# Performance work log

Measured on AMD Instinct MI355X. Metric: run time of the kernel, lower is better.

Reference implementation:

```python
import jax, jax.numpy as jnp
import numpy as np

EPS = 1e-6
NEG = -10000.0

def compute_alibi_slopes(n_head):
    # standard ALiBi slopes for power-of-two head counts: 2^{-8(i+1)/n}
    start = 2.0 ** (-8.0 / n_head)
    return jnp.asarray([start ** (i + 1) for i in range(n_head)], dtype=jnp.float32)

def setup_inputs() -> dict:
    key = jax.random.key(0)
    k1, k2, k3 = jax.random.split(key, 3)
    B, T, C, H = 2, 2048, 1024, 16
    x = jax.random.normal(k1, (B, T, C), dtype=jnp.float32)
    # torch nn.Linear weights are [out_features, in_features]
    w_qkv = jax.random.normal(k2, (3 * C, C), dtype=jnp.float32) * (C ** -0.5)
    w_out = jax.random.normal(k3, (C, C), dtype=jnp.float32) * (C ** -0.5)
    alibi_slopes = compute_alibi_slopes(H)
    return {"x": x, "w_qkv": w_qkv, "w_out": w_out, "alibi_slopes": alibi_slopes}

def rational_softmax(scores, eps=EPS):
    # algebraic sigmoid 0.5*(1 + x/sqrt(1+x^2)) normalized along last axis
    num = 0.5 * (1.0 + scores * jax.lax.rsqrt(1.0 + scores * scores))
    return num / (jnp.sum(num, axis=-1, keepdims=True) + eps)

def reference(x, w_qkv, w_out, alibi_slopes):
    B, T, C = x.shape
    H = alibi_slopes.shape[0]
    D = C // H
    scale = 1.0 / jnp.sqrt(jnp.float32(D))
    qkv = (x @ w_qkv.T).reshape(B, T, 3, H, D)
    qkv = jnp.transpose(qkv, (2, 0, 3, 1, 4))  # [3,B,H,T,D]
    q, k, v = qkv[0], qkv[1], qkv[2]
    scores = jnp.einsum("bhtd,bhsd->bhts", q, k) * scale  # [B,H,T,T]
    pos = jnp.arange(T)
    rel = pos[:, None] - pos[None, :]  # [T,T]
    alibi = -jnp.abs(rel).astype(jnp.float32) * alibi_slopes[None, :, None, None]
    scores = scores + alibi
    causal = rel < 0  # strictly upper triangle (j > i)
    scores = jnp.where(causal[None, None], NEG, scores)
    probs = rational_softmax(scores, EPS)
    out = jnp.einsum("bhts,bhsd->bhtd", probs, v)  # [B,H,T,D]
    out = jnp.transpose(out, (0, 2, 1, 3)).reshape(B, T, C)
    return out @ w_out.T
```

## Files before the change

kernel.cpp:

```cpp
#include <hip/hip_runtime.h>
#include <stdint.h>

typedef __attribute__((ext_vector_type(8))) short bf16x8;
typedef __attribute__((ext_vector_type(4))) float f32x4;
typedef __attribute__((ext_vector_type(16))) float f32x16;

#define MFMA_16x16x32(a, b, c) __builtin_amdgcn_mfma_f32_16x16x32_bf16((a), (b), (c), 0, 0, 0)
#define MFMA_32x32x16(a, b, c) __builtin_amdgcn_mfma_f32_32x32x16_bf16((a), (b), (c), 0, 0, 0)

__device__ __forceinline__ short f2bf(float f) {
  union { float f; uint32_t u; } x;
  x.f = f;
  uint32_t r = x.u + 0x7fffu + ((x.u >> 16) & 1u);
  return (short)(r >> 16);
}

__device__ __forceinline__ uint32_t cvt_pk_bf16(float lo, float hi) {
  uint32_t r;
  asm("v_cvt_pk_bf16_f32 %0, %1, %2" : "=v"(r) : "v"(lo), "v"(hi));
  return r;
}

__device__ __forceinline__ void gload_lds16(const short* g, short* l) {
  __builtin_amdgcn_global_load_lds(
      (const __attribute__((address_space(1))) void*)g,
      (__attribute__((address_space(3))) void*)l, 16, 0, 0);
}

__global__ __launch_bounds__(256) void cast_all(const float* __restrict__ x,
                                                const float* __restrict__ wq,
                                                const float* __restrict__ wo,
                                                short* __restrict__ xb,
                                                short* __restrict__ wqb,
                                                short* __restrict__ wob) {
  int i = blockIdx.x * 256 + threadIdx.x;
  const float* s;
  short* d;
  int off;
  float sc = 1.0f;
  if (i < 524288) { s = x; d = xb; off = i; }
  else if (i < 917504) {
    s = wq; d = wqb; off = i - 524288;
    if (off < 131072) sc = 0.125f;
  }
  else { s = wo; d = wob; off = i - 917504; }
  const float4* sp = (const float4*)s;
  float4 v0 = sp[(size_t)off * 2 + 0];
  float4 v1 = sp[(size_t)off * 2 + 1];
  bf16x8 o;
  o[0] = f2bf(v0.x * sc); o[1] = f2bf(v0.y * sc); o[2] = f2bf(v0.z * sc); o[3] = f2bf(v0.w * sc);
  o[4] = f2bf(v1.x * sc); o[5] = f2bf(v1.y * sc); o[6] = f2bf(v1.z * sc); o[7] = f2bf(v1.w * sc);
  *(bf16x8*)(d + (size_t)off * 8) = o;
}

template <int OUT_BF16>
__global__ __launch_bounds__(512, 2) void gemm256(const short* __restrict__ A,
                                                  const short* __restrict__ B,
                                                  void* __restrict__ Cp,
                                                  int M, int N, int K, int ntN) {
  __shared__ short Al[2][2][128 * 64];
  __shared__ short Bl[2][2][128 * 64];

  const int tid = threadIdx.x;
  const int wv = tid >> 6, lane = tid & 63;
  const int wr = wv >> 2, wc = wv & 3;
  const int lrow = lane & 15, kgrp = lane >> 4;
  const int l3 = lrow & 7;
  const int ck0 = ((kgrp ^ l3)) * 8;
  const int ck1 = ((kgrp ^ l3) ^ 4) * 8;

  const int nwg = gridDim.x;
  const int orig = blockIdx.x;
  const int wg = (orig & 7) * (nwg >> 3) + (orig >> 3);
  const int by = wg / ntN, bx = wg % ntN;
  const int row0 = by * 256, col0 = bx * 256;

  const int r_ = tid >> 3;
  const int cs_ = ((tid & 7) ^ (r_ & 7)) * 8;

  const int NT = K >> 6;
  const int NI = NT >> 1;
  const int NTm1 = NT - 1;

  auto stgA = [&](int slot, int h, int j, int kt) {
    gload_lds16(A + (size_t)(row0 + h * 128 + j * 64 + r_) * K + kt * 64 + cs_,
                &Al[slot][h][j * 4096 + wv * 512]);
  };
  auto stgB = [&](int slot, int h, int j, int kt) {
    gload_lds16(B + (size_t)(col0 + h * 128 + j * 64 + r_) * K + kt * 64 + cs_,
                &Bl[slot][h][j * 4096 + wv * 512]);
  };

  f32x4 acc[8][4] = {};

  const int boff = ((wc & 1) * 64 + lrow) * 64;
  const int bh = wc >> 1;

  stgB(0, 0, 0, 0); stgB(0, 0, 1, 0); stgB(0, 1, 0, 0); stgB(0, 1, 1, 0);
  stgA(0, 0, 0, 0); stgA(0, 0, 1, 0); stgA(0, 1, 0, 0); stgA(0, 1, 1, 0);
  stgB(1, 0, 0, 1); stgB(1, 0, 1, 1); stgB(1, 1, 0, 1); stgB(1, 1, 1, 1);
  asm volatile("s_waitcnt vmcnt(4)" ::: "memory");
  __builtin_amdgcn_s_barrier();

  for (int i = 0; i < NI; ++i) {
    const int ktB1 = (2 * i + 1);
    const int ktP2 = (2 * i + 2 > NTm1) ? NTm1 : 2 * i + 2;
    const int ktP3 = (2 * i + 3 > NTm1) ? NTm1 : 2 * i + 3;
#pragma unroll
    for (int s = 0; s < 2; ++s) {
      bf16x8 bfr[4][2];
#pragma unroll
      for (int q = 0; q < 4; ++q) {
        if (q == 0) {
#pragma unroll
          for (int n = 0; n < 4; ++n) {
            bfr[n][0] = *(const bf16x8*)(&Bl[s][bh][boff + n * 1024 + ck0]);
            bfr[n][1] = *(const bf16x8*)(&Bl[s][bh][boff + n * 1024 + ck1]);
          }
        }
        bf16x8 afr[2][2];
#pragma unroll
        for (int mm = 0; mm < 2; ++mm) {
          const int m = q * 2 + mm;
          afr[mm][0] = *(const bf16x8*)(&Al[s][wr][lrow * 64 + m * 1024 + ck0]);
          afr[mm][1] = *(const bf16x8*)(&Al[s][wr][lrow * 64 + m * 1024 + ck1]);
        }
        if (s == 0) {
          if (q == 0) { stgA(1, 0, 0, ktB1); stgA(1, 0, 1, ktB1); stgA(1, 1, 0, ktB1); stgA(1, 1, 1, ktB1); }
          else if (q == 1) { stgB(0, 0, 0, ktP2); stgB(0, 0, 1, ktP2); }
          else if (q == 2) { stgB(0, 1, 0, ktP2); stgB(0, 1, 1, ktP2); }
        } else {
          if (q == 0) { stgA(0, 0, 0, ktP2); stgA(0, 0, 1, ktP2); stgA(0, 1, 0, ktP2); stgA(0, 1, 1, ktP2); }
          else if (q == 1) { stgB(1, 0, 0, ktP3); stgB(1, 0, 1, ktP3); }
          else if (q == 2) { stgB(1, 1, 0, ktP3); stgB(1, 1, 1, ktP3); }
        }
        __builtin_amdgcn_sched_barrier(0);
        __builtin_amdgcn_s_barrier();
        asm volatile("s_waitcnt lgkmcnt(0)" ::: "memory");
        __builtin_amdgcn_sched_barrier(0);
        __builtin_amdgcn_s_setprio(1);
#pragma unroll
        for (int mm = 0; mm < 2; ++mm)
#pragma unroll
          for (int n = 0; n < 4; ++n)
#pragma unroll
            for (int kk = 0; kk < 2; ++kk)
              acc[q * 2 + mm][n] = MFMA_16x16x32(afr[mm][kk], bfr[n][kk], acc[q * 2 + mm][n]);
        __builtin_amdgcn_s_setprio(0);
        __builtin_amdgcn_sched_barrier(0);
        if (q == 3) {
          asm volatile("s_waitcnt vmcnt(4)" ::: "memory");
        }
        __builtin_amdgcn_s_barrier();
      }
    }
  }

  asm volatile("s_waitcnt vmcnt(0)" ::: "memory");

#pragma unroll
  for (int m = 0; m < 8; ++m) {
    const int grow = row0 + wr * 128 + m * 16 + kgrp * 4;
#pragma unroll
    for (int n = 0; n < 4; ++n) {
      const int gcol = col0 + wc * 64 + n * 16 + lrow;
#pragma unroll
      for (int j = 0; j < 4; ++j) {
        const size_t off = (size_t)(grow + j) * N + gcol;
        if (OUT_BF16) ((short*)Cp)[off] = f2bf(acc[m][n][j]);
        else          ((float*)Cp)[off] = acc[m][n][j];
      }
    }
  }
}

template <int OUT_BF16>
__global__ __launch_bounds__(256, 4) void gemm_bt64(const short* __restrict__ A,
                                                    const short* __restrict__ B,
                                                    void* __restrict__ Cp,
                                                    int M, int N, int K) {
  __shared__ short As[64 * 64];
  __shared__ short Bs[128 * 64];
  const int tid = threadIdx.x;
  const int wave = tid >> 6, lane = tid & 63;
  const int wr = wave >> 1, wc = wave & 1;
  const int row0 = blockIdx.y * 64, col0 = blockIdx.x * 128;
  const int lrow = lane & 15;
  const int kgrp = lane >> 4;
  const int l3 = lrow & 7;

  const int r_ = tid >> 3;
  const int cs_ = ((tid & 7) ^ (r_ & 7)) * 8;

  f32x4 acc[2][4] = {};

  for (int k0 = 0; k0 < K; k0 += 64) {
#pragma unroll
    for (int it = 0; it < 2; ++it)
      gload_lds16(A + (size_t)(row0 + it * 32 + r_) * K + k0 + cs_,
                  As + (it * 256 + wave * 64) * 8);
#pragma unroll
    for (int it = 0; it < 4; ++it)
      gload_lds16(B + (size_t)(col0 + it * 32 + r_) * K + k0 + cs_,
                  Bs + (it * 256 + wave * 64) * 8);
    __syncthreads();
#pragma unroll
    for (int kk = 0; kk < 2; ++kk) {
      const int ck = ((kk * 4 + kgrp) ^ l3) * 8;
      bf16x8 a[2], b[4];
#pragma unroll
      for (int m = 0; m < 2; ++m)
        a[m] = *(const bf16x8*)(As + (wr * 32 + m * 16 + lrow) * 64 + ck);
#pragma unroll
      for (int n = 0; n < 4; ++n)
        b[n] = *(const bf16x8*)(Bs + (wc * 64 + n * 16 + lrow) * 64 + ck);
#pragma unroll
      for (int m = 0; m < 2; ++m)
#pragma unroll
        for (int n = 0; n < 4; ++n)
          acc[m][n] = MFMA_16x16x32(a[m], b[n], acc[m][n]);
    }
    __syncthreads();
  }

#pragma unroll
  for (int m = 0; m < 2; ++m) {
    int rbase = row0 + wr * 32 + m * 16 + kgrp * 4;
#pragma unroll
    for (int n = 0; n < 4; ++n) {
      int col = col0 + wc * 64 + n * 16 + lrow;
#pragma unroll
      for (int j = 0; j < 4; ++j) {
        size_t off = (size_t)(rbase + j) * N + col;
        if (OUT_BF16) ((short*)Cp)[off] = f2bf(acc[m][n][j]);
        else          ((float*)Cp)[off] = acc[m][n][j];
      }
    }
  }
}

__global__ __launch_bounds__(256) void transpose_v(const short* __restrict__ qkv,
                                                   short* __restrict__ vt) {
  const int T = 2048;
  __shared__ short sm[64][72];
  const int bh = blockIdx.y, h = bh & 15, b = bh >> 4;
  const int t0 = blockIdx.x * 64;
  const int tid = threadIdx.x;
#pragma unroll
  for (int p = 0; p < 2; ++p) {
    int idx = p * 256 + tid;
    int tl = idx >> 3, d0 = (idx & 7) * 8;
    bf16x8 v = *(const bf16x8*)(qkv + (b * T + t0 + tl) * 3072 + 2048 + h * 64 + d0);
    *(bf16x8*)(&sm[tl][d0]) = v;
  }
  __syncthreads();
#pragma unroll
  for (int p = 0; p < 2; ++p) {
    int idx = p * 256 + tid;
    int d = idx >> 3, ts0 = (idx & 7) * 8;
    bf16x8 o;
#pragma unroll
    for (int j = 0; j < 8; ++j) o[j] = sm[ts0 + j][d];
    *(bf16x8*)(vt + (bh * 64 + d) * T + t0 + ts0) = o;
  }
}

template <bool DIAG>
__device__ __forceinline__ void attn_sub(
    const short* __restrict__ Kb, const short* __restrict__ Vb,
    const bf16x8 (&qf)[4], const f32x16& crun,
    f32x16& acc0, f32x16& acc1, float (&den4)[4],
    int l31, int hi, int shalf, int mbits) {
  const int krow = l31 >> 1;
  const int kc0 = (l31 & 1) * 8 + hi;
  const int ss = shalf;
  __builtin_amdgcn_s_setprio(1);
  const bf16x8 kf0 = *(const bf16x8*)(Kb + (ss * 16 + krow) * 128 + (kc0 ^ krow) * 8);
  f32x16 s = MFMA_32x32x16(kf0, qf[0], crun);
#pragma unroll
  for (int kkd = 1; kkd < 4; ++kkd) {
    const bf16x8 kf = *(const bf16x8*)(Kb + (ss * 16 + krow) * 128 +
                                       ((kc0 + kkd * 2) ^ krow) * 8);
    s = MFMA_32x32x16(kf, qf[kkd], s);
  }
  __builtin_amdgcn_s_setprio(0);
  float nm[16];
#pragma unroll
  for (int v = 0; v < 16; ++v) {
    float x = s[v];
    if (DIAG) x = ((mbits >> v) & 1) ? -10000.0f : x;
    float t = fmaf(x, x, 1.0f);
    float num = fmaf(x * __builtin_amdgcn_rsqf(t), 0.5f, 0.5f);
    den4[v & 3] += num;
    nm[v] = num;
  }
#pragma unroll
  for (int k1 = 0; k1 < 2; ++k1) {
    union { uint32_t u[4]; bf16x8 v8; } pu;
#pragma unroll
    for (int w01 = 0; w01 < 2; ++w01) {
      uint32_t c0 = cvt_pk_bf16(nm[2 * w01 + 8 * k1], nm[2 * w01 + 8 * k1 + 1]);
      uint32_t c1 = cvt_pk_bf16(nm[2 * w01 + 8 * k1 + 4], nm[2 * w01 + 8 * k1 + 5]);
      asm volatile("v_permlane32_swap_b32 %0, %1" : "+v"(c0), "+v"(c1));
      pu.u[w01] = c0;
      pu.u[w01 + 2] = c1;
    }
    const int vsw = ((((l31 & 1) * 8) + ss * 4 + k1 * 2 + hi) ^ krow) * 8;
    const bf16x8 vf0 = *(const bf16x8*)(Vb + krow * 128 + vsw);
    const bf16x8 vf1 = *(const bf16x8*)(Vb + (16 + krow) * 128 + vsw);
    __builtin_amdgcn_s_setprio(1);
    acc0 = MFMA_32x32x16(pu.v8, vf0, acc0);
    acc1 = MFMA_32x32x16(pu.v8, vf1, acc1);
    __builtin_amdgcn_s_setprio(0);
  }
}

__global__ __launch_bounds__(256, 3) void attn_kernel(const short* __restrict__ qkv,
                                                      const short* __restrict__ vt,
                                                      const float* __restrict__ slopes,
                                                      short* __restrict__ attn_out) {
  const int T = 2048, C = 1024, C3 = 3072;
  __shared__ short Kl[3][4096];
  __shared__ short Vl[3][4096];
  __shared__ float denm[64];

  const int tid = threadIdx.x, wv = tid >> 6, lane = tid & 63;
  const int l31 = lane & 31, hi = lane >> 5;
  const int wg = blockIdx.x;
  const int bh = (wg & 7) + ((wg >> 3) & 3) * 8;
  const int qi = 31 - (wg >> 5);
  const int b = bh >> 4, h = bh & 15;
  const int qsub = wv >> 1, shalf = wv & 1;
  const float slope = slopes[h];
  const float s64 = slope * 64.0f;

  const int W = (int)(45.0f / (64.0f * slope)) + 2;
  const int kt0 = (qi - W > 0) ? (qi - W) : 0;

  int mbits = 0;
#pragma unroll
  for (int v = 0; v < 16; ++v) {
    int s32 = (v & 3) + 8 * (v >> 2) + 4 * hi;
    if (s32 > l31) mbits |= (1 << v);
  }
  int koff[2], voff[2];
#pragma unroll
  for (int p = 0; p < 2; ++p) {
    int idx = p * 256 + tid;
    int rho = idx >> 4, u = idx & 15, c = u ^ (rho & 15);
    koff[p] = (2 * rho + (c >> 3)) * C3 + (c & 7) * 8;
    voff[p] = (2 * rho + (c >> 3)) * T + (c & 7) * 8;
  }
  const short* kbase = qkv + (size_t)b * T * C3 + C + h * 64;
  const short* vbase = vt + (size_t)bh * 64 * T;

  auto STAGE = [&](int bufi, int kt) {
#pragma unroll
    for (int p = 0; p < 2; ++p)
      gload_lds16(kbase + (size_t)kt * 64 * C3 + koff[p], &Kl[bufi][(p * 256 + wv * 64) * 8]);
#pragma unroll
    for (int p = 0; p < 2; ++p)
      gload_lds16(vbase + kt * 64 + voff[p], &Vl[bufi][(p * 256 + wv * 64) * 8]);
  };

  STAGE(0, kt0);
  STAGE(1, (kt0 + 1 > qi) ? qi : kt0 + 1);

  const int qg = qi * 64 + qsub * 32 + l31;
  bf16x8 qf[4];
#pragma unroll
  for (int ks = 0; ks < 4; ++ks)
    qf[ks] = *(const bf16x8*)(qkv + (size_t)(b * T + qg) * C3 + h * 64 + ks * 16 + hi * 8);

  f32x16 crun;
#pragma unroll
  for (int v = 0; v < 16; ++v) {
    int s32 = (v & 3) + 8 * (v >> 2) + 4 * hi;
    crun[v] = slope * (float)(s32 - l31 + 32 * (shalf - qsub) + 64 * (kt0 - qi));
  }

  f32x16 acc0 = {}, acc1 = {};
  float den4[4] = {0.f, 0.f, 0.f, 0.f};

  int cA = 0, cS = 2;
  for (int kt = kt0; kt < qi; ++kt) {
    const int kt2 = (kt + 2 > qi) ? qi : kt + 2;
    STAGE(cS, kt2);
    asm volatile("s_waitcnt vmcnt(8)" ::: "memory");
    __builtin_amdgcn_s_barrier();
    attn_sub<false>(Kl[cA], Vl[cA], qf, crun, acc0, acc1, den4, l31, hi, shalf, mbits);
#pragma unroll
    for (int v = 0; v < 16; ++v) crun[v] += s64;
    __builtin_amdgcn_s_barrier();
    cA = (cA == 2) ? 0 : cA + 1;
    cS = (cS == 2) ? 0 : cS + 1;
  }
  asm volatile("s_waitcnt vmcnt(4)" ::: "memory");
  __builtin_amdgcn_s_barrier();
  if (!(qsub == 0 && shalf == 1)) {
    if (qsub == 1 && shalf == 0)
      attn_sub<false>(Kl[cA], Vl[cA], qf, crun, acc0, acc1, den4, l31, hi, shalf, mbits);
    else
      attn_sub<true>(Kl[cA], Vl[cA], qf, crun, acc0, acc1, den4, l31, hi, shalf, mbits);
  }
  __syncthreads();

  float den = (den4[0] + den4[1]) + (den4[2] + den4[3]);
  den += __shfl_xor(den, 32);

  if (shalf == 1) {
    float* mp = (float*)(qsub == 0 ? &Kl[cS][0] : &Vl[cS][0]);
#pragma unroll
    for (int i = 0; i < 16; ++i) {
      mp[i * 64 + lane] = acc0[i];
      mp[(16 + i) * 64 + lane] = acc1[i];
    }
    if (hi == 0) denm[qsub * 32 + l31] = den;
  }
  __syncthreads();

  if (shalf == 0) {
    const float* mp = (const float*)(qsub == 0 ? &Kl[cS][0] : &Vl[cS][0]);
    den += denm[qsub * 32 + l31];
#pragma unroll
    for (int i = 0; i < 16; ++i) {
      acc0[i] += mp[i * 64 + lane];
      acc1[i] += mp[(16 + i) * 64 + lane];
    }
    short* obase = attn_out + (size_t)(b * T + qi * 64 + qsub * 32) * C + h * 64;
#pragma unroll
    for (int v = 0; v < 16; ++v) {
      int ql = (v & 3) + 8 * (v >> 2) + 4 * hi;
      float dv = __int_as_float(__builtin_amdgcn_ds_bpermute(ql << 2, __float_as_int(den)));
      float r = __builtin_amdgcn_rcpf(dv + 1e-6f);
      obase[(size_t)ql * C + l31] = f2bf(acc0[v] * r);
      obase[(size_t)ql * C + 32 + l31] = f2bf(acc1[v] * r);
    }
  }
}

extern "C" void kernel_launch(void* const* d_in, const int* in_sizes, int n_in,
                              void* d_out, int out_size, void* d_ws, size_t ws_size,
                              hipStream_t stream) {
  const float* x      = (const float*)d_in[0];
  const float* w_qkv  = (const float*)d_in[1];
  const float* w_out  = (const float*)d_in[2];
  const float* slopes = (const float*)d_in[3];

  const int B = 2, T = 2048, C = 1024;
  const int M = B * T;
  const int N1 = 3 * C;

  char* ws = (char*)d_ws;
  short* x_bf    = (short*)(ws);
  short* wqkv_bf = (short*)(ws + 8388608);
  short* wout_bf = (short*)(ws + 14680064);
  short* qkv_bf  = (short*)(ws + 16777216);
  short* vt_bf   = (short*)(ws + 41943040);
  short* ao_bf   = (short*)(ws + 50331648);

  cast_all<<<4096, 256, 0, stream>>>(x, w_qkv, w_out, x_bf, wqkv_bf, wout_bf);

  gemm256<1><<<dim3((M / 256) * (N1 / 256)), 512, 0, stream>>>(x_bf, wqkv_bf, qkv_bf,
                                                               M, N1, C, N1 / 256);

  transpose_v<<<dim3(T / 64, 32), 256, 0, stream>>>(qkv_bf, vt_bf);

  attn_kernel<<<1024, 256, 0, stream>>>(qkv_bf, vt_bf, slopes, ao_bf);

  gemm_bt64<0><<<dim3(C / 128, M / 64), 256, 0, stream>>>(ao_bf, wout_bf, (float*)d_out, M, C, C);
}
```

Before: 101.8 us.

## Double-buffer GEMM K-loop, use one barrier per attention tile, pair heads per XCD

```diff
diff --git a/kernel.cpp b/kernel.cpp
--- a/kernel.cpp
+++ b/kernel.cpp
@@ -179,8 +179,8 @@
                                                     const short* __restrict__ B,
                                                     void* __restrict__ Cp,
                                                     int M, int N, int K) {
-  __shared__ short As[64 * 64];
-  __shared__ short Bs[128 * 64];
+  __shared__ short As[2][64 * 64];
+  __shared__ short Bs[2][128 * 64];
   const int tid = threadIdx.x;
   const int wave = tid >> 6, lane = tid & 63;
   const int wr = wave >> 1, wc = wave & 1;
@@ -192,36 +192,51 @@
   const int r_ = tid >> 3;
   const int cs_ = ((tid & 7) ^ (r_ & 7)) * 8;
 
+  const int NT = K >> 6;
+
+  auto STG = [&](int buf, int kt) {
+#pragma unroll
+    for (int it = 0; it < 2; ++it)
+      gload_lds16(A + (size_t)(row0 + it * 32 + r_) * K + kt * 64 + cs_,
+                  &As[buf][(it * 256 + wave * 64) * 8]);
+#pragma unroll
+    for (int it = 0; it < 4; ++it)
+      gload_lds16(B + (size_t)(col0 + it * 32 + r_) * K + kt * 64 + cs_,
+                  &Bs[buf][(it * 256 + wave * 64) * 8]);
+  };
+
   f32x4 acc[2][4] = {};
 
-  for (int k0 = 0; k0 < K; k0 += 64) {
-#pragma unroll
-    for (int it = 0; it < 2; ++it)
-      gload_lds16(A + (size_t)(row0 + it * 32 + r_) * K + k0 + cs_,
-                  As + (it * 256 + wave * 64) * 8);
-#pragma unroll
-    for (int it = 0; it < 4; ++it)
-      gload_lds16(B + (size_t)(col0 + it * 32 + r_) * K + k0 + cs_,
-                  Bs + (it * 256 + wave * 64) * 8);
-    __syncthreads();
+  STG(0, 0);
+
+  for (int kt = 0; kt < NT; ++kt) {
+    __builtin_amdgcn_s_barrier();
+    __builtin_amdgcn_sched_barrier(0);
+    const int ktn = (kt + 1 >= NT) ? NT - 1 : kt + 1;
+    STG((kt + 1) & 1, ktn);
+    asm volatile("s_waitcnt vmcnt(6)" ::: "memory");
+    __builtin_amdgcn_sched_barrier(0);
+    const short* Ab = As[kt & 1];
+    const short* Bb = Bs[kt & 1];
 #pragma unroll
     for (int kk = 0; kk < 2; ++kk) {
       const int ck = ((kk * 4 + kgrp) ^ l3) * 8;
       bf16x8 a[2], b[4];
 #pragma unroll
       for (int m = 0; m < 2; ++m)
-        a[m] = *(const bf16x8*)(As + (wr * 32 + m * 16 + lrow) * 64 + ck);
+        a[m] = *(const bf16x8*)(Ab + (wr * 32 + m * 16 + lrow) * 64 + ck);
 #pragma unroll
       for (int n = 0; n < 4; ++n)
-        b[n] = *(const bf16x8*)(Bs + (wc * 64 + n * 16 + lrow) * 64 + ck);
+        b[n] = *(const bf16x8*)(Bb + (wc * 64 + n * 16 + lrow) * 64 + ck);
 #pragma unroll
       for (int m = 0; m < 2; ++m)
 #pragma unroll
         for (int n = 0; n < 4; ++n)
           acc[m][n] = MFMA_16x16x32(a[m], b[n], acc[m][n]);
     }
-    __syncthreads();
-  }
+  }
+
+  asm volatile("s_waitcnt vmcnt(0)" ::: "memory");
 
 #pragma unroll
   for (int m = 0; m < 2; ++m) {
@@ -315,6 +330,9 @@
   }
 }
 
+__device__ __constant__ int HPAIR[8][2] = {
+  {15, 0}, {14, 1}, {13, 2}, {12, 3}, {11, 4}, {10, 5}, {9, 6}, {8, 7}};
+
 __global__ __launch_bounds__(256, 3) void attn_kernel(const short* __restrict__ qkv,
                                                       const short* __restrict__ vt,
                                                       const float* __restrict__ slopes,
@@ -327,9 +345,12 @@
   const int tid = threadIdx.x, wv = tid >> 6, lane = tid & 63;
   const int l31 = lane & 31, hi = lane >> 5;
   const int wg = blockIdx.x;
-  const int bh = (wg & 7) + ((wg >> 3) & 3) * 8;
-  const int qi = 31 - (wg >> 5);
-  const int b = bh >> 4, h = bh & 15;
+  const int xcd = wg & 7, j = wg >> 3;
+  const int bhsel = j & 3;
+  const int qi = 31 - (j >> 2);
+  const int h = HPAIR[xcd][bhsel & 1];
+  const int b = bhsel >> 1;
+  const int bh = b * 16 + h;
   const int qsub = wv >> 1, shalf = wv & 1;
   const float slope = slopes[h];
   const float s64 = slope * 64.0f;
@@ -363,14 +384,15 @@
       gload_lds16(vbase + kt * 64 + voff[p], &Vl[bufi][(p * 256 + wv * 64) * 8]);
   };
 
+  const int qg = qi * 64 + qsub * 32 + l31;
+  bf16x8 qf[4];
+#pragma unroll
+  for (int ks = 0; ks < 4; ++ks)
+    qf[ks] = *(const bf16x8*)(qkv + (size_t)(b * T + qg) * C3 + h * 64 + ks * 16 + hi * 8);
+  __builtin_amdgcn_sched_barrier(0);
+
   STAGE(0, kt0);
   STAGE(1, (kt0 + 1 > qi) ? qi : kt0 + 1);
-
-  const int qg = qi * 64 + qsub * 32 + l31;
-  bf16x8 qf[4];
-#pragma unroll
-  for (int ks = 0; ks < 4; ++ks)
-    qf[ks] = *(const bf16x8*)(qkv + (size_t)(b * T + qg) * C3 + h * 64 + ks * 16 + hi * 8);
 
   f32x16 crun;
 #pragma unroll
@@ -382,18 +404,17 @@
   f32x16 acc0 = {}, acc1 = {};
   float den4[4] = {0.f, 0.f, 0.f, 0.f};
 
-  int cA = 0, cS = 2;
+  int cA = 0;
   for (int kt = kt0; kt < qi; ++kt) {
-    const int kt2 = (kt + 2 > qi) ? qi : kt + 2;
-    STAGE(cS, kt2);
-    asm volatile("s_waitcnt vmcnt(8)" ::: "memory");
+    asm volatile("s_waitcnt vmcnt(4)" ::: "memory");
     __builtin_amdgcn_s_barrier();
+    __builtin_amdgcn_sched_barrier(0);
+    int cS = cA + 2; if (cS >= 3) cS -= 3;
+    STAGE(cS, (kt + 2 > qi) ? qi : kt + 2);
     attn_sub<false>(Kl[cA], Vl[cA], qf, crun, acc0, acc1, den4, l31, hi, shalf, mbits);
 #pragma unroll
     for (int v = 0; v < 16; ++v) crun[v] += s64;
-    __builtin_amdgcn_s_barrier();
     cA = (cA == 2) ? 0 : cA + 1;
-    cS = (cS == 2) ? 0 : cS + 1;
   }
   asm volatile("s_waitcnt vmcnt(4)" ::: "memory");
   __builtin_amdgcn_s_barrier();
@@ -405,11 +426,12 @@
   }
   __syncthreads();
 
+  int sc = cA + 1; if (sc >= 3) sc -= 3;
   float den = (den4[0] + den4[1]) + (den4[2] + den4[3]);
   den += __shfl_xor(den, 32);
 
   if (shalf == 1) {
-    float* mp = (float*)(qsub == 0 ? &Kl[cS][0] : &Vl[cS][0]);
+    float* mp = (float*)(qsub == 0 ? &Kl[sc][0] : &Vl[sc][0]);
 #pragma unroll
     for (int i = 0; i < 16; ++i) {
       mp[i * 64 + lane] = acc0[i];
@@ -420,7 +442,7 @@
   __syncthreads();
 
   if (shalf == 0) {
-    const float* mp = (const float*)(qsub == 0 ? &Kl[cS][0] : &Vl[cS][0]);
+    const float* mp = (const float*)(qsub == 0 ? &Kl[sc][0] : &Vl[sc][0]);
     den += denm[qsub * 32 + l31];
 #pragma unroll
     for (int i = 0; i < 16; ++i) {
```

Measured after the change: 102.3 us. Within noise of the previous version (+0.5%).
